# Kernel optimization log

Measured on AMD Instinct MI355X. Metric: run time of the kernel, lower is better.

Reference implementation:

```python
import jax, jax.numpy as jnp
import numpy as np

H = 16
DH = 64


def _apply_rotary(x, cos, sin):
    # x: [b, h, s, d]; cos/sin: [s, d//2] -> broadcast to [1, 1, s, d//2]
    x1 = x[..., ::2]
    x2 = x[..., 1::2]
    c = cos[None, None]
    s = sin[None, None]
    rot = jnp.stack([x1 * c - x2 * s, x1 * s + x2 * c], axis=-1)
    return rot.reshape(x.shape)


def setup_inputs() -> dict:
    key = jax.random.key(0)
    ks = jax.random.split(key, 7)
    dim = 1024
    std = 0.02
    x = jax.random.normal(ks[0], (2, 2048, dim), dtype=jnp.float32)
    persistent = jax.random.normal(ks[1], (2, 16, dim), dtype=jnp.float32)
    memory = jax.random.normal(ks[2], (2, 64, dim), dtype=jnp.float32)
    Wq = jax.random.normal(ks[3], (dim, dim), dtype=jnp.float32) * std
    Wk = jax.random.normal(ks[4], (dim, dim), dtype=jnp.float32) * std
    Wv = jax.random.normal(ks[5], (dim, dim), dtype=jnp.float32) * std
    Wo = jax.random.normal(ks[6], (dim, dim), dtype=jnp.float32) * std
    return {"x": x, "persistent": persistent, "memory": memory,
            "Wq": Wq, "Wk": Wk, "Wv": Wv, "Wo": Wo}


def reference(x, persistent, memory, Wq, Wk, Wv, Wo):
    b, L, dim = x.shape
    P = persistent.shape[1] + memory.shape[1]  # prefix_len
    full_x = jnp.concatenate([persistent, memory, x], axis=1)  # [b, P+L, dim]
    S = full_x.shape[1]
    scale = DH ** -0.5

    def proj(W):
        y = full_x @ W.T  # [b, S, dim]
        return y.reshape(b, S, H, DH).transpose(0, 2, 1, 3)  # [b, H, S, DH]

    q = proj(Wq)
    k = proj(Wk)
    v = proj(Wv)

    # RoPE only on the main (input) segment, positions starting at 0.
    pos = jnp.arange(L, dtype=jnp.float32)
    inv_freq = 1.0 / (10000.0 ** (jnp.arange(0, DH, 2, dtype=jnp.float32) / DH))
    freqs = pos[:, None] * inv_freq[None, :]  # [L, DH//2]
    cos, sin = jnp.cos(freqs), jnp.sin(freqs)

    q_main = _apply_rotary(q[:, :, P:], cos, sin)  # [b, H, L, DH]
    k = jnp.concatenate([k[:, :, :P], _apply_rotary(k[:, :, P:], cos, sin)], axis=2)

    # Only main-segment query rows affect the returned output (output[:, P:]).
    # Mask for main queries: prefix keys fully visible; causal within main.
    qi = jnp.arange(L)[:, None]
    kj = jnp.arange(S)[None, :]
    mask = (kj < P) | ((kj - P) <= qi)  # [L, S]

    scores = jnp.einsum('bhqd,bhkd->bhqk', q_main, k) * scale  # [b, H, L, S]
    scores = jnp.where(mask[None, None], scores, -jnp.inf)
    attn = jax.nn.softmax(scores, axis=-1)
    out = jnp.einsum('bhqk,bhkd->bhqd', attn, v)  # [b, H, L, DH]
    out = out.transpose(0, 2, 1, 3).reshape(b, L, dim)
    return out @ Wo.T
```

## Files before the change

kernel.cpp:

```cpp
#include <hip/hip_runtime.h>
#include <math.h>

#define BB    2
#define LL    2048
#define DIM   1024
#define NH    16
#define DHD   64
#define NPER  16
#define NMEM  64
#define PFX   80
#define SS    2128
#define MQKV  (BB*SS)
#define NQKV  3072
#define MOUT  (BB*LL)

typedef __attribute__((ext_vector_type(4)))  float f32x4;
typedef __attribute__((ext_vector_type(16))) float f32x16;
typedef __attribute__((ext_vector_type(8)))  short bf16x8;
typedef unsigned short u16;
typedef unsigned int   u32;

union I4B8 { int4 i; bf16x8 v; };

__device__ __forceinline__ u16 f2bf(float x) {
    union { float f; u32 u; } v; v.f = x;
    return (u16)((v.u + 0x7fffu + ((v.u >> 16) & 1u)) >> 16);
}
__device__ __forceinline__ u32 cvtpk(float lo, float hi) {
    u32 r; asm("v_cvt_pk_bf16_f32 %0, %1, %2" : "=v"(r) : "v"(lo), "v"(hi));
    return r;
}
__device__ __forceinline__ void gload_lds16(const void* g, void* l) {
    __builtin_amdgcn_global_load_lds(
        (__attribute__((address_space(1))) void*)(g),
        (__attribute__((address_space(3))) void*)(l), 16, 0, 0);
}

#define BARRIER()  __builtin_amdgcn_s_barrier()
#define VMCNT8()   asm volatile("s_waitcnt vmcnt(8)")

__global__ __launch_bounds__(256)
void prep_kernel(const float* __restrict__ x,  const float* __restrict__ pe,
                 const float* __restrict__ me, const float* __restrict__ Wq,
                 const float* __restrict__ Wk, const float* __restrict__ Wv,
                 const float* __restrict__ Wo,
                 u16* __restrict__ xbf, u16* __restrict__ wqkv,
                 u16* __restrict__ wobf,
                 float* __restrict__ ropeC, float* __restrict__ ropeS)
{
    const int nthr = gridDim.x * blockDim.x;
    const int t0   = blockIdx.x * blockDim.x + threadIdx.x;

    for (int g = t0; g < MQKV * (DIM / 4); g += nthr) {
        int d4  = g & 255;
        int row = g >> 8;
        int b   = row >= SS;
        int s   = row - b * SS;
        const float* src;
        if (s < NPER)     src = pe + ((size_t)(b * NPER + s)) * DIM;
        else if (s < PFX) src = me + ((size_t)(b * NMEM + (s - NPER))) * DIM;
        else              src = x  + ((size_t)(b * LL   + (s - PFX)))  * DIM;
        float4 v = *reinterpret_cast<const float4*>(src + d4 * 4);
        ushort4 o; o.x = f2bf(v.x); o.y = f2bf(v.y); o.z = f2bf(v.z); o.w = f2bf(v.w);
        *reinterpret_cast<ushort4*>(xbf + (size_t)g * 4) = o;
    }
    for (int g = t0; g < NQKV * (DIM / 4); g += nthr) {
        int row = g >> 8;
        const float* src = (row < 1024) ? (Wq + (size_t)row * DIM)
                         : (row < 2048) ? (Wk + (size_t)(row - 1024) * DIM)
                         :                (Wv + (size_t)(row - 2048) * DIM);
        float4 v = *reinterpret_cast<const float4*>(src + (g & 255) * 4);
        ushort4 o; o.x = f2bf(v.x); o.y = f2bf(v.y); o.z = f2bf(v.z); o.w = f2bf(v.w);
        *reinterpret_cast<ushort4*>(wqkv + (size_t)g * 4) = o;
    }
    for (int g = t0; g < DIM * (DIM / 4); g += nthr) {
        float4 v = *reinterpret_cast<const float4*>(Wo + (size_t)g * 4);
        ushort4 o; o.x = f2bf(v.x); o.y = f2bf(v.y); o.z = f2bf(v.z); o.w = f2bf(v.w);
        *reinterpret_cast<ushort4*>(wobf + (size_t)g * 4) = o;
    }
    for (int i = t0; i < LL * 32; i += nthr) {
        int pos = i >> 5, fi = i & 31;
        float ang = (float)pos * exp2f(-(float)fi * 0.41524101186092029f);
        ropeC[i] = cosf(ang);
        ropeS[i] = sinf(ang);
    }
}

__device__ __forceinline__ void stage_half8(const u16* __restrict__ src, int grow0,
                                            int rmax, int k0, short* ldsbase, int tid)
{
#pragma unroll
    for (int rr = 0; rr < 2; ++rr) {
        int t   = tid + rr * 512;
        int row = t >> 3;
        int c   = t & 7;
        int g = grow0 + row; if (g > rmax) g = rmax;
        gload_lds16(src + (size_t)g * DIM + k0 + ((c ^ (row & 7)) << 3),
                    ldsbase + (tid >> 6) * 512 + rr * 4096);
    }
}

__device__ __forceinline__ bf16x8 ldsfrag(const short* hb, int row, int kbyte)
{
    int byte = (row * 128 + kbyte) ^ ((row & 7) << 4);
    I4B8 t;
    t.i = *reinterpret_cast<const int4*>(reinterpret_cast<const char*>(hb) + byte);
    return t.v;
}

__global__ __launch_bounds__(512, 1)
void qkv_gemm8(const u16* __restrict__ X, const u16* __restrict__ Wq3,
               const float* __restrict__ ropeC, const float* __restrict__ ropeS,
               u16* __restrict__ qb, u16* __restrict__ kb, u16* __restrict__ vb)
{
    __shared__ short Xs[2][16384] __attribute__((aligned(16)));
    __shared__ short Ws[2][16384] __attribute__((aligned(16)));

    const int tid  = threadIdx.x;
    const int lane = tid & 63;
    const int wid  = tid >> 6;
    const int wm   = wid >> 2;
    const int wn   = wid & 3;
    const int bm   = blockIdx.x * 256;
    const int bn   = blockIdx.y * 256;

    f32x4 acc[8][4];
#pragma unroll
    for (int r = 0; r < 8; ++r)
#pragma unroll
        for (int c = 0; c < 4; ++c) acc[r][c] = (f32x4)(0.f);

    stage_half8(X,   bm,       MQKV - 1, 0,  &Xs[0][0],    tid);
    stage_half8(X,   bm + 128, MQKV - 1, 0,  &Xs[0][8192], tid);
    stage_half8(Wq3, bn,       NQKV - 1, 0,  &Ws[0][0],    tid);
    stage_half8(Wq3, bn + 128, NQKV - 1, 0,  &Ws[0][8192], tid);
    stage_half8(X,   bm,       MQKV - 1, 64, &Xs[1][0],    tid);
    stage_half8(X,   bm + 128, MQKV - 1, 64, &Xs[1][8192], tid);
    stage_half8(Wq3, bn,       NQKV - 1, 64, &Ws[1][0],    tid);
    stage_half8(Wq3, bn + 128, NQKV - 1, 64, &Ws[1][8192], tid);
    VMCNT8();
    BARRIER();

    const int frow = lane & 15;
    const int fkb  = (lane >> 4) * 16;
    const int wrow = (wn & 1) * 64;
    const short* XhA[2] = { &Xs[0][0] + wm * 8192,        &Xs[1][0] + wm * 8192 };
    const short* WhA[2] = { &Ws[0][0] + (wn >> 1) * 8192, &Ws[1][0] + (wn >> 1) * 8192 };

    for (int it = 0; it < 8; ++it) {
        int ksA = it * 128 + 128; if (ksA >= 1024) ksA = 0;
        int ksB = it * 128 + 192; if (ksB >= 1024) ksB = 64;
#pragma unroll
        for (int sub = 0; sub < 2; ++sub) {
            const short* Xh = XhA[sub];
            const short* Wh = WhA[sub];
            const int kst = sub ? ksB : ksA;
            short* XsN = &Xs[sub][0];
            short* WsN = &Ws[sub][0];
            bf16x8 xfA[4][2], xfB[4][2], wfA[2][2], wfB[2][2];

#pragma unroll
            for (int r = 0; r < 4; ++r)
#pragma unroll
                for (int ks = 0; ks < 2; ++ks)
                    xfA[r][ks] = ldsfrag(Xh, r * 16 + frow, ks * 64 + fkb);
#pragma unroll
            for (int c = 0; c < 2; ++c)
#pragma unroll
                for (int ks = 0; ks < 2; ++ks)
                    wfA[c][ks] = ldsfrag(Wh, wrow + c * 16 + frow, ks * 64 + fkb);
            BARRIER();
            __builtin_amdgcn_s_setprio(1);
#pragma unroll
            for (int r = 0; r < 4; ++r)
#pragma unroll
                for (int c = 0; c < 2; ++c)
#pragma unroll
                    for (int ks = 0; ks < 2; ++ks)
                        acc[r][c] = __builtin_amdgcn_mfma_f32_16x16x32_bf16(
                            wfA[c][ks], xfA[r][ks], acc[r][c], 0, 0, 0);
            __builtin_amdgcn_s_setprio(0);
            BARRIER();

#pragma unroll
            for (int c = 0; c < 2; ++c)
#pragma unroll
                for (int ks = 0; ks < 2; ++ks)
                    wfB[c][ks] = ldsfrag(Wh, wrow + 32 + c * 16 + frow, ks * 64 + fkb);
            BARRIER();
            __builtin_amdgcn_s_setprio(1);
#pragma unroll
            for (int r = 0; r < 4; ++r)
#pragma unroll
                for (int c = 0; c < 2; ++c)
#pragma unroll
                    for (int ks = 0; ks < 2; ++ks)
                        acc[r][c + 2] = __builtin_amdgcn_mfma_f32_16x16x32_bf16(
                            wfB[c][ks], xfA[r][ks], acc[r][c + 2], 0, 0, 0);
            __builtin_amdgcn_s_setprio(0);
            BARRIER();

#pragma unroll
            for (int r = 0; r < 4; ++r)
#pragma unroll
                for (int ks = 0; ks < 2; ++ks)
                    xfB[r][ks] = ldsfrag(Xh, 64 + r * 16 + frow, ks * 64 + fkb);
            stage_half8(Wq3, bn,       NQKV - 1, kst, WsN,        tid);
            stage_half8(Wq3, bn + 128, NQKV - 1, kst, WsN + 8192, tid);
            BARRIER();
            __builtin_amdgcn_s_setprio(1);
#pragma unroll
            for (int r = 0; r < 4; ++r)
#pragma unroll
                for (int c = 0; c < 2; ++c)
#pragma unroll
                    for (int ks = 0; ks < 2; ++ks)
                        acc[r + 4][c] = __builtin_amdgcn_mfma_f32_16x16x32_bf16(
                            wfA[c][ks], xfB[r][ks], acc[r + 4][c], 0, 0, 0);
            __builtin_amdgcn_s_setprio(0);
            BARRIER();

            stage_half8(X, bm,       MQKV - 1, kst, XsN,        tid);
            stage_half8(X, bm + 128, MQKV - 1, kst, XsN + 8192, tid);
            BARRIER();
            __builtin_amdgcn_s_setprio(1);
#pragma unroll
            for (int r = 0; r < 4; ++r)
#pragma unroll
                for (int c = 0; c < 2; ++c)
#pragma unroll
                    for (int ks = 0; ks < 2; ++ks)
                        acc[r + 4][c + 2] = __builtin_amdgcn_mfma_f32_16x16x32_bf16(
                            wfB[c][ks], xfB[r][ks], acc[r + 4][c + 2], 0, 0, 0);
            __builtin_amdgcn_s_setprio(0);
            VMCNT8();
            BARRIER();
        }
    }

    const int cbase = bn + wn * 64 + ((lane >> 4) << 2);
    const int rbase = bm + wm * 128 + (lane & 15);
    const int which = bn >> 10;

#pragma unroll
    for (int xr = 0; xr < 8; ++xr) {
        const int row = rbase + xr * 16;
        if (row >= MQKV) continue;
        const int b = row >= SS;
        const int s = row - b * SS;
#pragma unroll
        for (int wc = 0; wc < 4; ++wc) {
            const int c0 = cbase + wc * 16;
            float v0 = acc[xr][wc][0], v1 = acc[xr][wc][1];
            float v2 = acc[xr][wc][2], v3 = acc[xr][wc][3];
            const int nn = c0 & 1023;
            const int h  = nn >> 6;
            const int dh = nn & 63;
            if (which != 2 && s >= PFX) {
                const int pos = s - PFX;
                float2 cs = *reinterpret_cast<const float2*>(ropeC + pos * 32 + (dh >> 1));
                float2 sn = *reinterpret_cast<const float2*>(ropeS + pos * 32 + (dh >> 1));
                float t0 = v0 * cs.x - v1 * sn.x;
                v1 = v0 * sn.x + v1 * cs.x; v0 = t0;
                float t2 = v2 * cs.y - v3 * sn.y;
                v3 = v2 * sn.y + v3 * cs.y; v2 = t2;
            }
            ushort4 o;
            o.x = f2bf(v0); o.y = f2bf(v1); o.z = f2bf(v2); o.w = f2bf(v3);
            if (which == 0) {
                if (s >= PFX)
                    *reinterpret_cast<ushort4*>(
                        &qb[(((size_t)b * NH + h) * LL + (s - PFX)) * DHD + dh]) = o;
            } else if (which == 1) {
                *reinterpret_cast<ushort4*>(
                    &kb[(((size_t)b * NH + h) * SS + s) * DHD + dh]) = o;
            } else {
                *reinterpret_cast<ushort4*>(
                    &vb[(((size_t)b * NH + h) * SS + s) * DHD + dh]) = o;
            }
        }
    }
}

__global__ __launch_bounds__(256)
void wo_gemm(const u16* __restrict__ A, const u16* __restrict__ Bw,
             float* __restrict__ outp)
{
    __shared__ short As[128 * 32] __attribute__((aligned(16)));
    __shared__ short Bs[128 * 32] __attribute__((aligned(16)));

    const int tid  = threadIdx.x;
    const int lane = tid & 63;
    const int wid  = tid >> 6;
    const int wr   = wid >> 1, wc = wid & 1;
    const int bm   = blockIdx.x * 128;
    const int bn   = blockIdx.y * 128;

    f32x4 acc[4][4];
#pragma unroll
    for (int m = 0; m < 4; ++m)
#pragma unroll
        for (int n = 0; n < 4; ++n) acc[m][n] = (f32x4)(0.f);

    const int r0 = wid * 32 + (lane >> 2);
    const int cc = (lane & 3) * 8;

    for (int k0 = 0; k0 < DIM; k0 += 32) {
        gload_lds16(A + (size_t)(bm + r0) * DIM + k0 + cc, As + wid * 1024);
        gload_lds16(A + (size_t)(bm + r0 + 16) * DIM + k0 + cc, As + wid * 1024 + 512);
        gload_lds16(Bw + (size_t)(bn + r0) * DIM + k0 + cc, Bs + wid * 1024);
        gload_lds16(Bw + (size_t)(bn + r0 + 16) * DIM + k0 + cc, Bs + wid * 1024 + 512);
        __syncthreads();

        bf16x8 wf[4], xf[4];
#pragma unroll
        for (int m = 0; m < 4; ++m)
            wf[m] = *reinterpret_cast<const bf16x8*>(
                Bs + (wr * 64 + m * 16 + (lane & 15)) * 32 + (lane >> 4) * 8);
#pragma unroll
        for (int n = 0; n < 4; ++n)
            xf[n] = *reinterpret_cast<const bf16x8*>(
                As + (wc * 64 + n * 16 + (lane & 15)) * 32 + (lane >> 4) * 8);
#pragma unroll
        for (int m = 0; m < 4; ++m)
#pragma unroll
            for (int n = 0; n < 4; ++n)
                acc[m][n] = __builtin_amdgcn_mfma_f32_16x16x32_bf16(
                    wf[m], xf[n], acc[m][n], 0, 0, 0);
        __syncthreads();
    }

    const int cbase = bn + wr * 64 + ((lane >> 4) << 2);
    const int rbase = bm + wc * 64 + (lane & 15);
#pragma unroll
    for (int n = 0; n < 4; ++n) {
        const int row = rbase + n * 16;
#pragma unroll
        for (int m = 0; m < 4; ++m) {
            const int c0 = cbase + m * 16;
            *reinterpret_cast<float4*>(&outp[(size_t)row * DIM + c0]) =
                make_float4(acc[m][n][0], acc[m][n][1], acc[m][n][2], acc[m][n][3]);
        }
    }
}

__device__ __forceinline__ void attn_load_tile(
    const u16* __restrict__ kb0, const u16* __restrict__ vb0,
    int j0, int tid, int vp, int vo,
    int4& k0r, int4& k1r, int4& v0r, int4& v1r)
{
    int key0 = tid >> 3,        o0 = tid & 7;
    int c1   = tid + 256;
    int key1 = c1 >> 3,         o1 = c1 & 7;
    int jg0 = j0 + key0; if (jg0 > SS - 1) jg0 = SS - 1;
    int jg1 = j0 + key1; if (jg1 > SS - 1) jg1 = SS - 1;
    k0r = *reinterpret_cast<const int4*>(kb0 + (size_t)jg0 * DHD + o0 * 8);
    k1r = *reinterpret_cast<const int4*>(kb0 + (size_t)jg1 * DHD + o1 * 8);
    int ja  = j0 + 2 * vp;     if (ja  > SS - 1) ja  = SS - 1;
    int jb2 = j0 + 2 * vp + 1; if (jb2 > SS - 1) jb2 = SS - 1;
    v0r = *reinterpret_cast<const int4*>(vb0 + (size_t)ja  * DHD + vo * 8);
    v1r = *reinterpret_cast<const int4*>(vb0 + (size_t)jb2 * DHD + vo * 8);
}

__global__ __launch_bounds__(256, 2)
void attn_mfma(const u16* __restrict__ qb, const u16* __restrict__ kb,
               const u16* __restrict__ vb, u16* __restrict__ ctx)
{
    __shared__ u16 Ks[64 * 64] __attribute__((aligned(16)));
    __shared__ u16 Vt[64 * 64] __attribute__((aligned(16)));
    __shared__ u16 Ot[4][32 * 72] __attribute__((aligned(16)));

    const int tid  = threadIdx.x;
    const int lane = tid & 63;
    const int wv   = tid >> 6;
    const int h    = lane >> 5;
    const int ql   = lane & 31;

    const int bh   = blockIdx.y;
    const int b    = bh >> 4;
    const int head = bh & 15;
    int qt = blockIdx.x;
    if (b) qt = 15 - qt;
    const int q0  = qt * 128;
    const int q0w = q0 + 32 * wv;

    const u16* qrow = qb + ((size_t)bh * LL + q0w + ql) * DHD;
    bf16x8 qf[4];
#pragma unroll
    for (int ks = 0; ks < 4; ++ks) {
        I4B8 t; t.i = *reinterpret_cast<const int4*>(qrow + ks * 16 + h * 8);
        qf[ks] = t.v;
    }

    f32x16 oa0 = (f32x16)(0.f), oa1 = (f32x16)(0.f);
    float m = -INFINITY, l = 0.f;

    const u16* kb0 = kb + (size_t)bh * SS * DHD;
    const u16* vb0 = vb + (size_t)bh * SS * DHD;

    const int ntiles   = (PFX + q0 + 128 + 63) / 64;
    const int wave_lim = PFX + q0w + 31;
    const int vp = tid & 31;
    const int vo = tid >> 5;

    int4 rk0, rk1, rv0, rv1;
    attn_load_tile(kb0, vb0, 0, tid, vp, vo, rk0, rk1, rv0, rv1);

    for (int kt = 0; kt < ntiles; ++kt) {
        const int j0 = kt * 64;

        {
            int key0 = tid >> 3, o0 = tid & 7;
            int c1 = tid + 256;
            int key1 = c1 >> 3, o1 = c1 & 7;
            *reinterpret_cast<int4*>((char*)Ks + ((key0 * 128 + o0 * 16) ^ ((key0 & 7) << 4))) = rk0;
            *reinterpret_cast<int4*>((char*)Ks + ((key1 * 128 + o1 * 16) ^ ((key1 & 7) << 4))) = rk1;
            const u16* pa = reinterpret_cast<const u16*>(&rv0);
            const u16* pb = reinterpret_cast<const u16*>(&rv1);
#pragma unroll
            for (int d = 0; d < 8; ++d) {
                u32 wpk = (u32)pa[d] | ((u32)pb[d] << 16);
                int dh = vo * 8 + d;
                *reinterpret_cast<u32*>((char*)Vt + ((dh * 128 + vp * 4) ^ ((d & 7) << 4))) = wpk;
            }
        }
        __syncthreads();

        int4 nk0, nk1, nv0, nv1;
        attn_load_tile(kb0, vb0, j0 + 64, tid, vp, vo, nk0, nk1, nv0, nv1);

        if (j0 <= wave_lim) {
            f32x16 s0 = (f32x16)(0.f), s1 = (f32x16)(0.f);
            __builtin_amdgcn_s_setprio(1);
#pragma unroll
            for (int ks = 0; ks < 4; ++ks) {
                I4B8 k0, k1;
                k0.i = *reinterpret_cast<const int4*>(
                    (const char*)Ks + (((ql) * 128 + ks * 32 + h * 16) ^ ((ql & 7) << 4)));
                k1.i = *reinterpret_cast<const int4*>(
                    (const char*)Ks + (((32 + ql) * 128 + ks * 32 + h * 16) ^ ((ql & 7) << 4)));
                s0 = __builtin_amdgcn_mfma_f32_32x32x16_bf16(k0.v, qf[ks], s0, 0, 0, 0);
                s1 = __builtin_amdgcn_mfma_f32_32x32x16_bf16(k1.v, qf[ks], s1, 0, 0, 0);
            }
            __builtin_amdgcn_s_setprio(0);
            float sv[32];
#pragma unroll
            for (int i = 0; i < 16; ++i) { sv[i] = s0[i] * 0.125f; sv[16 + i] = s1[i] * 0.125f; }
            if (j0 + 63 > PFX + q0w) {
                const int lim = PFX + q0w + ql - j0;
#pragma unroll
                for (int i = 0; i < 32; ++i) {
                    int koff = ((i >= 16) ? 32 : 0) + (i & 3) + 8 * ((i & 15) >> 2) + 4 * h;
                    if (koff > lim) sv[i] = -INFINITY;
                }
            }
            float mt = sv[0];
#pragma unroll
            for (int i = 1; i < 32; ++i) mt = fmaxf(mt, sv[i]);
            mt = fmaxf(mt, __shfl_xor(mt, 32));
            float mn = fmaxf(m, mt);
            float f = __expf(m - mn);
            m = mn;
            float ls = 0.f;
            u32 W0[8], W1[8];
#pragma unroll
            for (int i = 0; i < 8; ++i) {
                float pa = __expf(sv[2 * i] - m);
                float pb = __expf(sv[2 * i + 1] - m);
                ls += pa + pb;
                W0[i] = cvtpk(pa, pb);
            }
#pragma unroll
            for (int i = 0; i < 8; ++i) {
                float pa = __expf(sv[16 + 2 * i] - m);
                float pb = __expf(sv[16 + 2 * i + 1] - m);
                ls += pa + pb;
                W1[i] = cvtpk(pa, pb);
            }
            ls += __shfl_xor(ls, 32);
            l = l * f + ls;
#pragma unroll
            for (int i = 0; i < 16; ++i) { oa0[i] *= f; oa1[i] *= f; }

            __builtin_amdgcn_s_setprio(1);
#pragma unroll
            for (int ks = 0; ks < 4; ++ks) {
                const int a4 = (ks & 1) * 4;
                u32 A0, A1, A2, A3;
                if (ks < 2) { A0 = W0[a4]; A1 = W0[a4 + 1]; A2 = W0[a4 + 2]; A3 = W0[a4 + 3]; }
                else        { A0 = W1[a4]; A1 = W1[a4 + 1]; A2 = W1[a4 + 2]; A3 = W1[a4 + 3]; }
                asm volatile("v_permlane32_swap_b32 %0, %1" : "+v"(A0), "+v"(A2));
                asm volatile("v_permlane32_swap_b32 %0, %1" : "+v"(A1), "+v"(A3));
                I4B8 pf; pf.i = make_int4((int)A0, (int)A1, (int)A2, (int)A3);
                I4B8 vf0, vf1;
                vf0.i = *reinterpret_cast<const int4*>(
                    (const char*)Vt + (((ql) * 128 + ks * 32 + h * 16) ^ ((ql & 7) << 4)));
                vf1.i = *reinterpret_cast<const int4*>(
                    (const char*)Vt + (((32 + ql) * 128 + ks * 32 + h * 16) ^ ((ql & 7) << 4)));
                oa0 = __builtin_amdgcn_mfma_f32_32x32x16_bf16(vf0.v, pf.v, oa0, 0, 0, 0);
                oa1 = __builtin_amdgcn_mfma_f32_32x32x16_bf16(vf1.v, pf.v, oa1, 0, 0, 0);
            }
            __builtin_amdgcn_s_setprio(0);
        }
        __syncthreads();
        rk0 = nk0; rk1 = nk1; rv0 = nv0; rv1 = nv1;
    }

    const float inv = 1.f / l;
    u16* orow = &Ot[wv][ql * 72];
#pragma unroll
    for (int i = 0; i < 8; ++i) {
        u32 w0 = cvtpk(oa0[2 * i] * inv, oa0[2 * i + 1] * inv);
        u32 w1 = cvtpk(oa1[2 * i] * inv, oa1[2 * i + 1] * inv);
        int dh0 = ((2 * i) & 3) + 8 * ((2 * i) >> 2) + 4 * h;
        *reinterpret_cast<u32*>(&orow[dh0]) = w0;
        *reinterpret_cast<u32*>(&orow[32 + dh0]) = w1;
    }
    const int rr = lane >> 1, hh = lane & 1;
    const u16* src = &Ot[wv][rr * 72 + hh * 32];
    u16* dst = ctx + ((size_t)(b * LL + q0 + 32 * wv + rr)) * DIM + head * DHD + hh * 32;
#pragma unroll
    for (int i = 0; i < 4; ++i) {
        int4 t = *reinterpret_cast<const int4*>(src + i * 8);
        *reinterpret_cast<int4*>(dst + i * 8) = t;
    }
}

extern "C" void kernel_launch(void* const* d_in, const int* in_sizes, int n_in,
                              void* d_out, int out_size, void* d_ws, size_t ws_size,
                              hipStream_t stream)
{
    const float* x  = (const float*)d_in[0];
    const float* pe = (const float*)d_in[1];
    const float* me = (const float*)d_in[2];
    const float* Wq = (const float*)d_in[3];
    const float* Wk = (const float*)d_in[4];
    const float* Wv = (const float*)d_in[5];
    const float* Wo = (const float*)d_in[6];
    float* out = (float*)d_out;

    u16* xbf  = (u16*)d_ws;
    u16* wqkv = xbf + (size_t)MQKV * DIM;
    u16* wobf = wqkv + (size_t)NQKV * DIM;
    float* ropeC = (float*)(wobf + (size_t)DIM * DIM);
    float* ropeS = ropeC + LL * 32;
    u16* qbf = (u16*)(ropeS + LL * 32);
    u16* kbf = qbf + (size_t)BB * NH * LL * DHD;
    u16* vbf = kbf + (size_t)BB * NH * SS * DHD;
    u16* ctx = vbf + (size_t)BB * NH * SS * DHD;

    hipLaunchKernelGGL(prep_kernel, dim3(2048), dim3(256), 0, stream,
                       x, pe, me, Wq, Wk, Wv, Wo, xbf, wqkv, wobf, ropeC, ropeS);
    hipLaunchKernelGGL(qkv_gemm8, dim3((MQKV + 255) / 256, NQKV / 256), dim3(512), 0, stream,
                       xbf, wqkv, ropeC, ropeS, qbf, kbf, vbf);
    hipLaunchKernelGGL(attn_mfma, dim3(16, BB * NH), dim3(256), 0, stream,
                       qbf, kbf, vbf, ctx);
    hipLaunchKernelGGL(wo_gemm, dim3(MOUT / 128, DIM / 128), dim3(256), 0, stream,
                       ctx, wobf, out);
}
```

Measured before the change: 151.5 us.

## Fold softmax scale into Q, use exp2 with lazy rescale, swizzle blocks across XCDs

The Q projection epilogue now multiplies by scale*log2(e), so attention works in base 2 with exp2f and no per-score scaling. The online-softmax rescale of the accumulators is skipped unless some lane's max rises by more than a threshold, and the max reduction becomes a tree. All three kernels remap block indices so neighbouring tiles land on the same XCD for better L2 reuse. The goal is fewer ALU ops in the softmax loop and better cache locality. The cost is bounded growth in unnormalised exponentials and a more complex block mapping.

```diff
diff --git a/kernel.cpp b/kernel.cpp
--- a/kernel.cpp
+++ b/kernel.cpp
@@ -14,6 +14,8 @@
 #define NQKV  3072
 #define MOUT  (BB*LL)
 
+#define QSCALE 0.1803368842f
+
 typedef __attribute__((ext_vector_type(4)))  float f32x4;
 typedef __attribute__((ext_vector_type(16))) float f32x16;
 typedef __attribute__((ext_vector_type(8)))  short bf16x8;
@@ -121,8 +123,13 @@
     const int wid  = tid >> 6;
     const int wm   = wid >> 2;
     const int wn   = wid & 3;
-    const int bm   = blockIdx.x * 256;
-    const int bn   = blockIdx.y * 256;
+
+    const int lin  = blockIdx.y * 17 + blockIdx.x;
+    const int xcd  = lin & 7;
+    const int ii   = lin >> 3;
+    const int work = ((xcd < 4) ? xcd * 26 : 104 + (xcd - 4) * 25) + ii;
+    const int bm   = (work % 17) * 256;
+    const int bn   = (work / 17) * 256;
 
     f32x4 acc[8][4];
 #pragma unroll
@@ -265,6 +272,9 @@
                 float t2 = v2 * cs.y - v3 * sn.y;
                 v3 = v2 * sn.y + v3 * cs.y; v2 = t2;
             }
+            if (which == 0) {
+                v0 *= QSCALE; v1 *= QSCALE; v2 *= QSCALE; v3 *= QSCALE;
+            }
             ushort4 o;
             o.x = f2bf(v0); o.y = f2bf(v1); o.z = f2bf(v2); o.w = f2bf(v3);
             if (which == 0) {
@@ -293,8 +303,11 @@
     const int lane = tid & 63;
     const int wid  = tid >> 6;
     const int wr   = wid >> 1, wc = wid & 1;
-    const int bm   = blockIdx.x * 128;
-    const int bn   = blockIdx.y * 128;
+
+    const int lin = blockIdx.y * 32 + blockIdx.x;
+    const int swz = (lin & 7) * 32 + (lin >> 3);
+    const int bm  = (swz & 31) * 128;
+    const int bn  = (swz >> 5) * 128;
 
     f32x4 acc[4][4];
 #pragma unroll
@@ -376,10 +389,12 @@
     const int h    = lane >> 5;
     const int ql   = lane & 31;
 
-    const int bh   = blockIdx.y;
-    const int b    = bh >> 4;
+    const int lin = blockIdx.y * 16 + blockIdx.x;
+    const int swz = (lin & 7) * 64 + (lin >> 3);
+    const int bh  = swz >> 4;
+    const int b   = bh >> 4;
     const int head = bh & 15;
-    int qt = blockIdx.x;
+    int qt = swz & 15;
     if (b) qt = 15 - qt;
     const int q0  = qt * 128;
     const int q0w = q0 + 32 * wv;
@@ -443,44 +458,52 @@
                 s1 = __builtin_amdgcn_mfma_f32_32x32x16_bf16(k1.v, qf[ks], s1, 0, 0, 0);
             }
             __builtin_amdgcn_s_setprio(0);
-            float sv[32];
-#pragma unroll
-            for (int i = 0; i < 16; ++i) { sv[i] = s0[i] * 0.125f; sv[16 + i] = s1[i] * 0.125f; }
+
             if (j0 + 63 > PFX + q0w) {
                 const int lim = PFX + q0w + ql - j0;
 #pragma unroll
-                for (int i = 0; i < 32; ++i) {
-                    int koff = ((i >= 16) ? 32 : 0) + (i & 3) + 8 * ((i & 15) >> 2) + 4 * h;
-                    if (koff > lim) sv[i] = -INFINITY;
+                for (int i = 0; i < 16; ++i) {
+                    int k0f = (i & 3) + 8 * (i >> 2) + 4 * h;
+                    if (k0f > lim)      s0[i] = -INFINITY;
+                    if (32 + k0f > lim) s1[i] = -INFINITY;
                 }
             }
-            float mt = sv[0];
-#pragma unroll
-            for (int i = 1; i < 32; ++i) mt = fmaxf(mt, sv[i]);
-            mt = fmaxf(mt, __shfl_xor(mt, 32));
+            float tmx[16];
+#pragma unroll
+            for (int i = 0; i < 16; ++i) tmx[i] = fmaxf(s0[i], s1[i]);
+#pragma unroll
+            for (int st = 8; st > 0; st >>= 1)
+#pragma unroll
+                for (int i = 0; i < st; ++i) tmx[i] = fmaxf(tmx[i], tmx[i + st]);
+            float mt = fmaxf(tmx[0], __shfl_xor(tmx[0], 32));
+
             float mn = fmaxf(m, mt);
-            float f = __expf(m - mn);
-            m = mn;
+            if (!__all(mt - m <= 11.5f)) {
+                float f = exp2f(m - mn);
+                l *= f;
+#pragma unroll
+                for (int i = 0; i < 16; ++i) { oa0[i] *= f; oa1[i] *= f; }
+                m = mn;
+            }
+
             float ls = 0.f;
             u32 W0[8], W1[8];
 #pragma unroll
             for (int i = 0; i < 8; ++i) {
-                float pa = __expf(sv[2 * i] - m);
-                float pb = __expf(sv[2 * i + 1] - m);
+                float pa = exp2f(s0[2 * i] - m);
+                float pb = exp2f(s0[2 * i + 1] - m);
                 ls += pa + pb;
                 W0[i] = cvtpk(pa, pb);
             }
 #pragma unroll
             for (int i = 0; i < 8; ++i) {
-                float pa = __expf(sv[16 + 2 * i] - m);
-                float pb = __expf(sv[16 + 2 * i + 1] - m);
+                float pa = exp2f(s1[2 * i] - m);
+                float pb = exp2f(s1[2 * i + 1] - m);
                 ls += pa + pb;
                 W1[i] = cvtpk(pa, pb);
             }
             ls += __shfl_xor(ls, 32);
-            l = l * f + ls;
-#pragma unroll
-            for (int i = 0; i < 16; ++i) { oa0[i] *= f; oa1[i] *= f; }
+            l += ls;
 
             __builtin_amdgcn_s_setprio(1);
 #pragma unroll
```

Result: slower. 175.1 us (+15.5%).
